# Optimization experiments

Measured on AMD Instinct MI355X. Metric: run time of the kernel, lower is better.

The kernel has to match this reference:

```python
import jax, jax.numpy as jnp
import numpy as np

HIDDEN = 1024
ATTN = 1024
B, L = 16, 1024


def setup_inputs() -> dict:
    key = jax.random.key(0)
    ks = jax.random.split(key, 9)
    s = 1.0 / np.sqrt(HIDDEN)
    return {
        "meme_features": jax.random.normal(ks[0], (B, L, HIDDEN), jnp.float32),
        "text_features": jax.random.normal(ks[1], (B, L, HIDDEN), jnp.float32),
        "emoji_features": jax.random.normal(ks[2], (B, L, HIDDEN), jnp.float32),
        # nn.Linear params: weight [out, in], bias [out]
        "Wq": jax.random.uniform(ks[3], (ATTN, HIDDEN), jnp.float32, -s, s),
        "bq": jax.random.uniform(ks[4], (ATTN,), jnp.float32, -s, s),
        "Wk": jax.random.uniform(ks[5], (ATTN, HIDDEN), jnp.float32, -s, s),
        "bk": jax.random.uniform(ks[6], (ATTN,), jnp.float32, -s, s),
        "Wv": jax.random.uniform(ks[7], (ATTN, HIDDEN), jnp.float32, -s, s),
        "bv": jax.random.uniform(ks[8], (ATTN,), jnp.float32, -s, s),
    }


def reference(meme_features, text_features, emoji_features, Wq, bq, Wk, bk, Wv, bv):
    # Linear projections (x @ W^T + b)
    q = jnp.einsum("blh,ah->bla", meme_features, Wq) + bq   # [B, Lq, A]
    k = jnp.einsum("blh,ah->bla", text_features, Wk) + bk   # [B, Lk, A]
    v = jnp.einsum("blh,ah->bla", emoji_features, Wv) + bv  # [B, Lk, A]
    # NOTE: original module has NO 1/sqrt(d) scaling and NO mask.
    scores = jnp.einsum("bqa,bka->bqk", q, k)               # [B, Lq, Lk]
    weights = jax.nn.softmax(scores, axis=-1)
    return jnp.einsum("bqk,bka->bqa", weights, v)           # [B, Lq, A]
```

## Files before the change

### kernel.cpp

```cpp
#include <hip/hip_runtime.h>

typedef _Float16 half8_t __attribute__((ext_vector_type(8)));
typedef _Float16 half4_t __attribute__((ext_vector_type(4)));
typedef float floatx4 __attribute__((ext_vector_type(4)));
typedef float f32x16 __attribute__((ext_vector_type(16)));

__device__ inline void gload16(const void* g, void* l) {
  __builtin_amdgcn_global_load_lds(
      (const __attribute__((address_space(1))) unsigned int*)g,
      (__attribute__((address_space(3))) unsigned int*)l, 16, 0, 0);
}

constexpr int NT = 16;

__device__ inline void lda_frags2(const char* sA, int rb, const int* xk,
                                  half8_t af[2][4]) {
#pragma unroll
  for (int mp = 0; mp < 2; ++mp)
#pragma unroll
    for (int ks = 0; ks < 4; ++ks)
      af[mp][ks] = *(const half8_t*)(
          sA + (size_t)((rb + mp * 32) * 128 + xk[ks] * 16));
}

__device__ inline void ldb_frags2(const char* sB, int cb, const int* xk,
                                  half8_t bf[4]) {
#pragma unroll
  for (int ks = 0; ks < 4; ++ks)
    bf[ks] = *(const half8_t*)(sB + (size_t)(cb * 128 + xk[ks] * 16));
}

template <int MQ, int NI>
__device__ inline void mfma_quad(const half8_t af[2][4], const half8_t bf[4],
                                 f32x16 acc[4][2]) {
  __builtin_amdgcn_s_setprio(1);
#pragma unroll
  for (int mp = 0; mp < 2; ++mp)
#pragma unroll
    for (int ks = 0; ks < 4; ++ks)
      acc[MQ + mp][NI] = __builtin_amdgcn_mfma_f32_32x32x16_f16(
          af[mp][ks], bf[ks], acc[MQ + mp][NI], 0, 0, 0);
  __builtin_amdgcn_s_setprio(0);
}

__device__ inline void stage_half(const _Float16* __restrict__ X, long laneoff,
                                  int ldx, int u, char* opbase, int h,
                                  int wid) {
#pragma unroll
  for (int i = 0; i < 2; ++i) {
    const int c0 = h * 1024 + wid * 128 + i * 64;
    gload16(X + (long)(c0 >> 3) * ldx + u * 64 + laneoff,
            opbase + (size_t)c0 * 16);
  }
}

template <typename OT, int BIAS, int GX, int GY>
__global__ __launch_bounds__(512, 2) void gemm256(
    const _Float16* __restrict__ A, long As, int lda,
    const _Float16* __restrict__ B, long Bs, int ldb,
    OT* __restrict__ C, long Cs, int ldc, const float* __restrict__ bias,
    int biasStride) {
  __shared__ char smem[131072];

  const int id = blockIdx.x;
  const int chunk = gridDim.x >> 3;
  const int nid = (id & 7) * chunk + (id >> 3);
  const int bx = nid % GX;
  const int by = (nid / GX) % GY;
  const int bz = nid / (GX * GY);

  const int tid = threadIdx.x;
  const int lane = tid & 63;
  const int wid = tid >> 6;
  const int wr = wid >> 2;
  const int wc = wid & 3;
  const int lo = lane & 31;
  const int hi = lane >> 5;
  const int l7 = lane & 7;
  const int l8 = lane >> 3;
  const long laneA = (long)l8 * lda + ((l7 ^ l8) << 3);
  const long laneB = (long)l8 * ldb + ((l7 ^ l8) << 3);
  int xk[4];
#pragma unroll
  for (int ks = 0; ks < 4; ++ks) xk[ks] = (ks * 2 + hi) ^ l7;

  const long m0 = (long)by * 256;
  const long n0 = (long)bx * 256;
  const _Float16* Ab = A + (long)bz * As + m0 * (long)lda;
  const _Float16* Bb = B + (long)bz * Bs + n0 * (long)ldb;
  C += (long)bz * Cs;

  f32x16 acc[4][2] = {};
  half8_t af[2][4], bf0[4], bf1[4];

  char* sA0 = smem;
  char* sA1 = smem + 32768;
  char* sB0 = smem + 65536;
  char* sB1 = smem + 65536 + 32768;

  stage_half(Ab, laneA, lda, 0, sA0, 0, wid);
  stage_half(Bb, laneB, ldb, 0, sB0, 1, wid);
  stage_half(Ab, laneA, lda, 0, sA0, 1, wid);
  stage_half(Bb, laneB, ldb, 0, sB0, 0, wid);
  stage_half(Ab, laneA, lda, 1, sA1, 0, wid);
  stage_half(Bb, laneB, ldb, 1, sB1, 1, wid);
  stage_half(Ab, laneA, lda, 1, sA1, 1, wid);
  asm volatile("s_waitcnt vmcnt(6)" ::: "memory");
  __builtin_amdgcn_s_barrier();

  for (int t = 0; t < NT; ++t) {
    const int p = t & 1, q = p ^ 1;
    char* sAc = smem + p * 32768;
    char* sBc = smem + 65536 + p * 32768;
    char* sBq = smem + 65536 + q * 32768;
    const int u1 = (t + 1 < NT) ? t + 1 : NT - 1;
    const int u2 = (t + 2 < NT) ? t + 2 : NT - 1;

    lda_frags2(sAc, wr * 64 + lo, xk, af);
    ldb_frags2(sBc, wc * 32 + lo, xk, bf0);
    stage_half(Bb, laneB, ldb, u1, sBq, 0, wid);
    __builtin_amdgcn_s_barrier();
    asm volatile("s_waitcnt lgkmcnt(0)" ::: "memory");
    mfma_quad<0, 0>(af, bf0, acc);
    __builtin_amdgcn_s_barrier();

    ldb_frags2(sBc, 128 + wc * 32 + lo, xk, bf1);
    stage_half(Ab, laneA, lda, u2, sAc, 0, wid);
    __builtin_amdgcn_s_barrier();
    asm volatile("s_waitcnt lgkmcnt(0)" ::: "memory");
    mfma_quad<0, 1>(af, bf1, acc);
    __builtin_amdgcn_s_barrier();

    lda_frags2(sAc, 128 + wr * 64 + lo, xk, af);
    stage_half(Bb, laneB, ldb, u2, sBc, 1, wid);
    __builtin_amdgcn_s_barrier();
    asm volatile("s_waitcnt lgkmcnt(0)" ::: "memory");
    mfma_quad<2, 1>(af, bf1, acc);
    __builtin_amdgcn_s_barrier();

    stage_half(Ab, laneA, lda, u2, sAc, 1, wid);
    asm volatile("s_waitcnt vmcnt(6)" ::: "memory");
    __builtin_amdgcn_s_barrier();
    asm volatile("s_waitcnt lgkmcnt(0)" ::: "memory");
    mfma_quad<2, 0>(af, bf0, acc);
    __builtin_amdgcn_s_barrier();
  }

  asm volatile("s_waitcnt vmcnt(0)" ::: "memory");

#pragma unroll
  for (int mi = 0; mi < 4; ++mi) {
    const int r0 = (mi >> 1) * 128 + wr * 64 + (mi & 1) * 32 + 4 * hi;
#pragma unroll
    for (int ni = 0; ni < 2; ++ni) {
      const int cc = (int)n0 + ni * 128 + wc * 32 + lo;
#pragma unroll
      for (int e = 0; e < 16; ++e) {
        const long row = m0 + r0 + (e & 3) + 8 * (e >> 2);
        float v = acc[mi][ni][e];
        if constexpr (BIAS == 1) v += bias[bz * biasStride + cc];
        if constexpr (BIAS == 2) v += bias[(int)row];
        C[row * (long)ldc + cc] = (OT)v;
      }
    }
  }
}


__global__ __launch_bounds__(256) void convert_x(const float* __restrict__ x0,
                                                 const float* __restrict__ x1,
                                                 const float* __restrict__ x2,
                                                 _Float16* __restrict__ out) {
  int i = blockIdx.x * 256 + threadIdx.x;
  int t = i >> 22;
  int j = i & 4194303;
  const float* src = (t == 0) ? x0 : (t == 1) ? x1 : x2;
  floatx4 v = ((const floatx4*)src)[j];
  half4_t h = {(_Float16)v[0], (_Float16)v[1], (_Float16)v[2], (_Float16)v[3]};
  ((half4_t*)out)[i] = h;
}

__global__ __launch_bounds__(256) void convert_w(const float* __restrict__ Wq,
                                                 const float* __restrict__ Wk,
                                                 const float* __restrict__ Wv,
                                                 _Float16* __restrict__ out) {
  int i = blockIdx.x * 256 + threadIdx.x;
  int t = i >> 18;
  int j = i & 262143;
  const float* src = (t == 0) ? Wq : (t == 1) ? Wk : Wv;
  floatx4 v = ((const floatx4*)src)[j];
  half4_t h = {(_Float16)v[0], (_Float16)v[1], (_Float16)v[2], (_Float16)v[3]};
  ((half4_t*)out)[i] = h;
}

__global__ __launch_bounds__(256) void pack_bias(const float* __restrict__ bq,
                                                 const float* __restrict__ bk,
                                                 const float* __restrict__ bv,
                                                 float* __restrict__ out) {
  int b = blockIdx.x;
  const float* src = (b == 0) ? bq : (b == 1) ? bk : bv;
  ((floatx4*)out)[b * 256 + threadIdx.x] =
      ((const floatx4*)src)[threadIdx.x];
}

__global__ __launch_bounds__(256) void softmax_rows_h(_Float16* __restrict__ S) {
  long row = blockIdx.x;
  _Float16* Sr = S + row * 1024;
  int tid = threadIdx.x, lane = tid & 63, wid = tid >> 6;
  half4_t x = ((const half4_t*)Sr)[tid];
  float x0 = x[0], x1 = x[1], x2 = x[2], x3 = x[3];
  float mx = fmaxf(fmaxf(x0, x1), fmaxf(x2, x3));
#pragma unroll
  for (int off = 32; off > 0; off >>= 1) mx = fmaxf(mx, __shfl_xor(mx, off));
  __shared__ float redm[4];
  if (lane == 0) redm[wid] = mx;
  __syncthreads();
  mx = fmaxf(fmaxf(redm[0], redm[1]), fmaxf(redm[2], redm[3]));
  float e0 = __expf(x0 - mx), e1 = __expf(x1 - mx);
  float e2 = __expf(x2 - mx), e3 = __expf(x3 - mx);
  float s = e0 + e1 + e2 + e3;
#pragma unroll
  for (int off = 32; off > 0; off >>= 1) s += __shfl_xor(s, off);
  __shared__ float reds[4];
  if (lane == 0) reds[wid] = s;
  __syncthreads();
  s = reds[0] + reds[1] + reds[2] + reds[3];
  float inv = 1.0f / s;
  half4_t h = {(_Float16)(e0 * inv), (_Float16)(e1 * inv),
               (_Float16)(e2 * inv), (_Float16)(e3 * inv)};
  ((half4_t*)Sr)[tid] = h;
}

extern "C" void kernel_launch(void* const* d_in, const int* in_sizes, int n_in,
                              void* d_out, int out_size, void* d_ws,
                              size_t ws_size, hipStream_t stream) {
  (void)in_sizes; (void)n_in; (void)out_size; (void)ws_size;
  const float* meme  = (const float*)d_in[0];
  const float* text  = (const float*)d_in[1];
  const float* emoji = (const float*)d_in[2];
  const float* Wq = (const float*)d_in[3];
  const float* bq = (const float*)d_in[4];
  const float* Wk = (const float*)d_in[5];
  const float* bk = (const float*)d_in[6];
  const float* Wv = (const float*)d_in[7];
  const float* bv = (const float*)d_in[8];

  const long MB = 1024 * 1024;
  char* ws = (char*)d_ws;
  _Float16* hWq = (_Float16*)ws;
  float* pbias  = (float*)(ws + 6 * MB);
  _Float16* mh  = (_Float16*)(ws + 7 * MB);
  _Float16* th  = (_Float16*)(ws + 39 * MB);
  _Float16* eh  = (_Float16*)(ws + 71 * MB);
  _Float16* Qh  = (_Float16*)(ws + 103 * MB);
  _Float16* Kh  = (_Float16*)(ws + 135 * MB);
  _Float16* S   = mh;
  _Float16* Vt  = th;
  _Float16* hWv = hWq + 2 * MB;

  dim3 blk(256), blk5(512);
  convert_w<<<3072, blk, 0, stream>>>(Wq, Wk, Wv, hWq);
  pack_bias<<<3, blk, 0, stream>>>(bq, bk, bv, pbias);
  convert_x<<<49152, blk, 0, stream>>>(meme, text, emoji, mh);

  gemm256<_Float16, 1, 4, 64><<<dim3(512), blk5, 0, stream>>>(
      mh, 16777216, 1024, hWq, 1048576, 1024, Qh, 16777216, 1024, pbias, 1024);
  gemm256<_Float16, 2, 64, 4><<<dim3(256), blk5, 0, stream>>>(
      hWv, 0, 1024, eh, 0, 1024, Vt, 0, 16384, pbias + 2048, 0);
  gemm256<_Float16, 0, 4, 4><<<dim3(256), blk5, 0, stream>>>(
      Qh, 1048576, 1024, Kh, 1048576, 1024, S, 1048576, 1024, nullptr, 0);
  softmax_rows_h<<<16384, blk, 0, stream>>>(S);
  gemm256<float, 0, 4, 4><<<dim3(256), blk5, 0, stream>>>(
      S, 1048576, 1024, Vt, 1024, 16384, (float*)d_out, 1048576, 1024,
      nullptr, 0);
}
```

Measured before the change: 444.9 us.

## Replace 256x256 eight-wave GEMM with simpler 128x128 four-wave double-buffered GEMM

```diff
diff --git a/kernel.cpp b/kernel.cpp
--- a/kernel.cpp
+++ b/kernel.cpp
@@ -13,8 +13,8 @@
 
 constexpr int NT = 16;
 
-__device__ inline void lda_frags2(const char* sA, int rb, const int* xk,
-                                  half8_t af[2][4]) {
+__device__ inline void lda_frags(const char* sA, int rb, const int* xk,
+                                 half8_t af[2][4]) {
 #pragma unroll
   for (int mp = 0; mp < 2; ++mp)
 #pragma unroll
@@ -23,44 +23,33 @@
           sA + (size_t)((rb + mp * 32) * 128 + xk[ks] * 16));
 }
 
-__device__ inline void ldb_frags2(const char* sB, int cb, const int* xk,
-                                  half8_t bf[4]) {
-#pragma unroll
-  for (int ks = 0; ks < 4; ++ks)
-    bf[ks] = *(const half8_t*)(sB + (size_t)(cb * 128 + xk[ks] * 16));
-}
-
-template <int MQ, int NI>
-__device__ inline void mfma_quad(const half8_t af[2][4], const half8_t bf[4],
-                                 f32x16 acc[4][2]) {
-  __builtin_amdgcn_s_setprio(1);
-#pragma unroll
-  for (int mp = 0; mp < 2; ++mp)
+__device__ inline void ldb_frags(const char* sB, int cb, const int* xk,
+                                 half8_t bf[2][4]) {
+#pragma unroll
+  for (int np = 0; np < 2; ++np)
 #pragma unroll
     for (int ks = 0; ks < 4; ++ks)
-      acc[MQ + mp][NI] = __builtin_amdgcn_mfma_f32_32x32x16_f16(
-          af[mp][ks], bf[ks], acc[MQ + mp][NI], 0, 0, 0);
-  __builtin_amdgcn_s_setprio(0);
-}
-
-__device__ inline void stage_half(const _Float16* __restrict__ X, long laneoff,
-                                  int ldx, int u, char* opbase, int h,
-                                  int wid) {
-#pragma unroll
-  for (int i = 0; i < 2; ++i) {
-    const int c0 = h * 1024 + wid * 128 + i * 64;
+      bf[np][ks] = *(const half8_t*)(
+          sB + (size_t)((cb + np * 32) * 128 + xk[ks] * 16));
+}
+
+__device__ inline void stage_op(const _Float16* __restrict__ X, long laneoff,
+                                int ldx, int u, char* opbase, int wid) {
+#pragma unroll
+  for (int j = 0; j < 4; ++j) {
+    const int c0 = (wid * 4 + j) * 64;
     gload16(X + (long)(c0 >> 3) * ldx + u * 64 + laneoff,
             opbase + (size_t)c0 * 16);
   }
 }
 
 template <typename OT, int BIAS, int GX, int GY>
-__global__ __launch_bounds__(512, 2) void gemm256(
+__global__ __launch_bounds__(256) void gemm128(
     const _Float16* __restrict__ A, long As, int lda,
     const _Float16* __restrict__ B, long Bs, int ldb,
     OT* __restrict__ C, long Cs, int ldc, const float* __restrict__ bias,
     int biasStride) {
-  __shared__ char smem[131072];
+  __shared__ char smem[65536];
 
   const int id = blockIdx.x;
   const int chunk = gridDim.x >> 3;
@@ -72,8 +61,8 @@
   const int tid = threadIdx.x;
   const int lane = tid & 63;
   const int wid = tid >> 6;
-  const int wr = wid >> 2;
-  const int wc = wid & 3;
+  const int wr = wid >> 1;
+  const int wc = wid & 1;
   const int lo = lane & 31;
   const int hi = lane >> 5;
   const int l7 = lane & 7;
@@ -84,80 +73,60 @@
 #pragma unroll
   for (int ks = 0; ks < 4; ++ks) xk[ks] = (ks * 2 + hi) ^ l7;
 
-  const long m0 = (long)by * 256;
-  const long n0 = (long)bx * 256;
+  const long m0 = (long)by * 128;
+  const long n0 = (long)bx * 128;
   const _Float16* Ab = A + (long)bz * As + m0 * (long)lda;
   const _Float16* Bb = B + (long)bz * Bs + n0 * (long)ldb;
   C += (long)bz * Cs;
 
-  f32x16 acc[4][2] = {};
-  half8_t af[2][4], bf0[4], bf1[4];
-
-  char* sA0 = smem;
-  char* sA1 = smem + 32768;
-  char* sB0 = smem + 65536;
-  char* sB1 = smem + 65536 + 32768;
-
-  stage_half(Ab, laneA, lda, 0, sA0, 0, wid);
-  stage_half(Bb, laneB, ldb, 0, sB0, 1, wid);
-  stage_half(Ab, laneA, lda, 0, sA0, 1, wid);
-  stage_half(Bb, laneB, ldb, 0, sB0, 0, wid);
-  stage_half(Ab, laneA, lda, 1, sA1, 0, wid);
-  stage_half(Bb, laneB, ldb, 1, sB1, 1, wid);
-  stage_half(Ab, laneA, lda, 1, sA1, 1, wid);
-  asm volatile("s_waitcnt vmcnt(6)" ::: "memory");
+  f32x16 acc[2][2] = {};
+  half8_t af[2][4], bf[2][4];
+
+  stage_op(Ab, laneA, lda, 0, smem, wid);
+  stage_op(Bb, laneB, ldb, 0, smem + 32768, wid);
+  asm volatile("s_waitcnt vmcnt(0)" ::: "memory");
   __builtin_amdgcn_s_barrier();
 
   for (int t = 0; t < NT; ++t) {
     const int p = t & 1, q = p ^ 1;
-    char* sAc = smem + p * 32768;
-    char* sBc = smem + 65536 + p * 32768;
-    char* sBq = smem + 65536 + q * 32768;
+    char* sAp = smem + p * 16384;
+    char* sBp = smem + 32768 + p * 16384;
+    char* sAq = smem + q * 16384;
+    char* sBq = smem + 32768 + q * 16384;
     const int u1 = (t + 1 < NT) ? t + 1 : NT - 1;
-    const int u2 = (t + 2 < NT) ? t + 2 : NT - 1;
-
-    lda_frags2(sAc, wr * 64 + lo, xk, af);
-    ldb_frags2(sBc, wc * 32 + lo, xk, bf0);
-    stage_half(Bb, laneB, ldb, u1, sBq, 0, wid);
-    __builtin_amdgcn_s_barrier();
+
+    stage_op(Ab, laneA, lda, u1, sAq, wid);
+    stage_op(Bb, laneB, ldb, u1, sBq, wid);
+
+    lda_frags(sAp, wr * 64 + lo, xk, af);
+    ldb_frags(sBp, wc * 64 + lo, xk, bf);
     asm volatile("s_waitcnt lgkmcnt(0)" ::: "memory");
-    mfma_quad<0, 0>(af, bf0, acc);
-    __builtin_amdgcn_s_barrier();
-
-    ldb_frags2(sBc, 128 + wc * 32 + lo, xk, bf1);
-    stage_half(Ab, laneA, lda, u2, sAc, 0, wid);
-    __builtin_amdgcn_s_barrier();
-    asm volatile("s_waitcnt lgkmcnt(0)" ::: "memory");
-    mfma_quad<0, 1>(af, bf1, acc);
-    __builtin_amdgcn_s_barrier();
-
-    lda_frags2(sAc, 128 + wr * 64 + lo, xk, af);
-    stage_half(Bb, laneB, ldb, u2, sBc, 1, wid);
-    __builtin_amdgcn_s_barrier();
-    asm volatile("s_waitcnt lgkmcnt(0)" ::: "memory");
-    mfma_quad<2, 1>(af, bf1, acc);
-    __builtin_amdgcn_s_barrier();
-
-    stage_half(Ab, laneA, lda, u2, sAc, 1, wid);
-    asm volatile("s_waitcnt vmcnt(6)" ::: "memory");
-    __builtin_amdgcn_s_barrier();
-    asm volatile("s_waitcnt lgkmcnt(0)" ::: "memory");
-    mfma_quad<2, 0>(af, bf0, acc);
+
+    __builtin_amdgcn_s_setprio(1);
+#pragma unroll
+    for (int mp = 0; mp < 2; ++mp)
+#pragma unroll
+      for (int np = 0; np < 2; ++np)
+#pragma unroll
+        for (int ks = 0; ks < 4; ++ks)
+          acc[mp][np] = __builtin_amdgcn_mfma_f32_32x32x16_f16(
+              af[mp][ks], bf[np][ks], acc[mp][np], 0, 0, 0);
+    __builtin_amdgcn_s_setprio(0);
+
+    asm volatile("s_waitcnt vmcnt(0)" ::: "memory");
     __builtin_amdgcn_s_barrier();
   }
 
-  asm volatile("s_waitcnt vmcnt(0)" ::: "memory");
-
-#pragma unroll
-  for (int mi = 0; mi < 4; ++mi) {
-    const int r0 = (mi >> 1) * 128 + wr * 64 + (mi & 1) * 32 + 4 * hi;
-#pragma unroll
-    for (int ni = 0; ni < 2; ++ni) {
-      const int cc = (int)n0 + ni * 128 + wc * 32 + lo;
+#pragma unroll
+  for (int mp = 0; mp < 2; ++mp) {
+    const int r0 = wr * 64 + mp * 32 + 4 * hi;
+#pragma unroll
+    for (int np = 0; np < 2; ++np) {
+      const int cc = (int)n0 + wc * 64 + np * 32 + lo;
 #pragma unroll
       for (int e = 0; e < 16; ++e) {
         const long row = m0 + r0 + (e & 3) + 8 * (e >> 2);
-        float v = acc[mi][ni][e];
+        float v = acc[mp][np][e];
         if constexpr (BIAS == 1) v += bias[bz * biasStride + cc];
         if constexpr (BIAS == 2) v += bias[(int)row];
         C[row * (long)ldc + cc] = (OT)v;
@@ -258,19 +227,19 @@
   _Float16* Vt  = th;
   _Float16* hWv = hWq + 2 * MB;
 
-  dim3 blk(256), blk5(512);
+  dim3 blk(256);
   convert_w<<<3072, blk, 0, stream>>>(Wq, Wk, Wv, hWq);
   pack_bias<<<3, blk, 0, stream>>>(bq, bk, bv, pbias);
   convert_x<<<49152, blk, 0, stream>>>(meme, text, emoji, mh);
 
-  gemm256<_Float16, 1, 4, 64><<<dim3(512), blk5, 0, stream>>>(
+  gemm128<_Float16, 1, 8, 128><<<dim3(2048), blk, 0, stream>>>(
       mh, 16777216, 1024, hWq, 1048576, 1024, Qh, 16777216, 1024, pbias, 1024);
-  gemm256<_Float16, 2, 64, 4><<<dim3(256), blk5, 0, stream>>>(
+  gemm128<_Float16, 2, 128, 8><<<dim3(1024), blk, 0, stream>>>(
       hWv, 0, 1024, eh, 0, 1024, Vt, 0, 16384, pbias + 2048, 0);
-  gemm256<_Float16, 0, 4, 4><<<dim3(256), blk5, 0, stream>>>(
+  gemm128<_Float16, 0, 8, 8><<<dim3(1024), blk, 0, stream>>>(
       Qh, 1048576, 1024, Kh, 1048576, 1024, S, 1048576, 1024, nullptr, 0);
   softmax_rows_h<<<16384, blk, 0, stream>>>(S);
-  gemm256<float, 0, 4, 4><<<dim3(256), blk5, 0, stream>>>(
+  gemm128<float, 0, 8, 8><<<dim3(1024), blk, 0, stream>>>(
       S, 1048576, 1024, Vt, 1024, 16384, (float*)d_out, 1048576, 1024,
       nullptr, 0);
 }
```

Measured after the change: 466.0 us. 4.8% more time.

## Load all LDS fragments up front and collapse the per-tile pipeline to two phases

Applied to the files above, without the earlier changes.

```diff
diff --git a/kernel.cpp b/kernel.cpp
--- a/kernel.cpp
+++ b/kernel.cpp
@@ -13,33 +13,38 @@
 
 constexpr int NT = 16;
 
-__device__ inline void lda_frags2(const char* sA, int rb, const int* xk,
-                                  half8_t af[2][4]) {
-#pragma unroll
-  for (int mp = 0; mp < 2; ++mp)
+__device__ inline void lda_all(const char* sA, int wr, int lo, const int* xk,
+                               half8_t af[4][4]) {
+#pragma unroll
+  for (int mi = 0; mi < 4; ++mi) {
+    const int row = (mi >> 1) * 128 + wr * 64 + (mi & 1) * 32 + lo;
 #pragma unroll
     for (int ks = 0; ks < 4; ++ks)
-      af[mp][ks] = *(const half8_t*)(
-          sA + (size_t)((rb + mp * 32) * 128 + xk[ks] * 16));
-}
-
-__device__ inline void ldb_frags2(const char* sB, int cb, const int* xk,
-                                  half8_t bf[4]) {
+      af[mi][ks] = *(const half8_t*)(sA + (size_t)(row * 128 + xk[ks] * 16));
+  }
+}
+
+__device__ inline void ldb_all(const char* sB, int wc, int lo, const int* xk,
+                               half8_t bf[2][4]) {
+#pragma unroll
+  for (int ni = 0; ni < 2; ++ni) {
+    const int row = ni * 128 + wc * 32 + lo;
+#pragma unroll
+    for (int ks = 0; ks < 4; ++ks)
+      bf[ni][ks] = *(const half8_t*)(sB + (size_t)(row * 128 + xk[ks] * 16));
+  }
+}
+
+template <int NI>
+__device__ inline void mfma_col(const half8_t af[4][4], const half8_t bf[2][4],
+                                f32x16 acc[4][2]) {
+  __builtin_amdgcn_s_setprio(1);
 #pragma unroll
   for (int ks = 0; ks < 4; ++ks)
-    bf[ks] = *(const half8_t*)(sB + (size_t)(cb * 128 + xk[ks] * 16));
-}
-
-template <int MQ, int NI>
-__device__ inline void mfma_quad(const half8_t af[2][4], const half8_t bf[4],
-                                 f32x16 acc[4][2]) {
-  __builtin_amdgcn_s_setprio(1);
-#pragma unroll
-  for (int mp = 0; mp < 2; ++mp)
-#pragma unroll
-    for (int ks = 0; ks < 4; ++ks)
-      acc[MQ + mp][NI] = __builtin_amdgcn_mfma_f32_32x32x16_f16(
-          af[mp][ks], bf[ks], acc[MQ + mp][NI], 0, 0, 0);
+#pragma unroll
+    for (int mi = 0; mi < 4; ++mi)
+      acc[mi][NI] = __builtin_amdgcn_mfma_f32_32x32x16_f16(
+          af[mi][ks], bf[NI][ks], acc[mi][NI], 0, 0, 0);
   __builtin_amdgcn_s_setprio(0);
 }
 
@@ -91,7 +96,7 @@
   C += (long)bz * Cs;
 
   f32x16 acc[4][2] = {};
-  half8_t af[2][4], bf0[4], bf1[4];
+  half8_t af[4][4], bf[2][4];
 
   char* sA0 = smem;
   char* sA1 = smem + 32768;
@@ -99,50 +104,36 @@
   char* sB1 = smem + 65536 + 32768;
 
   stage_half(Ab, laneA, lda, 0, sA0, 0, wid);
-  stage_half(Bb, laneB, ldb, 0, sB0, 1, wid);
   stage_half(Ab, laneA, lda, 0, sA0, 1, wid);
   stage_half(Bb, laneB, ldb, 0, sB0, 0, wid);
+  stage_half(Bb, laneB, ldb, 0, sB0, 1, wid);
   stage_half(Ab, laneA, lda, 1, sA1, 0, wid);
+  stage_half(Ab, laneA, lda, 1, sA1, 1, wid);
   stage_half(Bb, laneB, ldb, 1, sB1, 1, wid);
-  stage_half(Ab, laneA, lda, 1, sA1, 1, wid);
   asm volatile("s_waitcnt vmcnt(6)" ::: "memory");
   __builtin_amdgcn_s_barrier();
 
   for (int t = 0; t < NT; ++t) {
     const int p = t & 1, q = p ^ 1;
-    char* sAc = smem + p * 32768;
-    char* sBc = smem + 65536 + p * 32768;
+    char* sAp = smem + p * 32768;
+    char* sBp = smem + 65536 + p * 32768;
     char* sBq = smem + 65536 + q * 32768;
     const int u1 = (t + 1 < NT) ? t + 1 : NT - 1;
     const int u2 = (t + 2 < NT) ? t + 2 : NT - 1;
 
-    lda_frags2(sAc, wr * 64 + lo, xk, af);
-    ldb_frags2(sBc, wc * 32 + lo, xk, bf0);
+    lda_all(sAp, wr, lo, xk, af);
+    ldb_all(sBp, wc, lo, xk, bf);
     stage_half(Bb, laneB, ldb, u1, sBq, 0, wid);
     __builtin_amdgcn_s_barrier();
     asm volatile("s_waitcnt lgkmcnt(0)" ::: "memory");
-    mfma_quad<0, 0>(af, bf0, acc);
+    mfma_col<0>(af, bf, acc);
     __builtin_amdgcn_s_barrier();
 
-    ldb_frags2(sBc, 128 + wc * 32 + lo, xk, bf1);
-    stage_half(Ab, laneA, lda, u2, sAc, 0, wid);
-    __builtin_amdgcn_s_barrier();
-    asm volatile("s_waitcnt lgkmcnt(0)" ::: "memory");
-    mfma_quad<0, 1>(af, bf1, acc);
-    __builtin_amdgcn_s_barrier();
-
-    lda_frags2(sAc, 128 + wr * 64 + lo, xk, af);
-    stage_half(Bb, laneB, ldb, u2, sBc, 1, wid);
-    __builtin_amdgcn_s_barrier();
-    asm volatile("s_waitcnt lgkmcnt(0)" ::: "memory");
-    mfma_quad<2, 1>(af, bf1, acc);
-    __builtin_amdgcn_s_barrier();
-
-    stage_half(Ab, laneA, lda, u2, sAc, 1, wid);
+    stage_half(Ab, laneA, lda, u2, sAp, 0, wid);
+    stage_half(Ab, laneA, lda, u2, sAp, 1, wid);
+    stage_half(Bb, laneB, ldb, u2, sBp, 1, wid);
+    mfma_col<1>(af, bf, acc);
     asm volatile("s_waitcnt vmcnt(6)" ::: "memory");
-    __builtin_amdgcn_s_barrier();
-    asm volatile("s_waitcnt lgkmcnt(0)" ::: "memory");
-    mfma_quad<2, 0>(af, bf0, acc);
     __builtin_amdgcn_s_barrier();
   }
 
```

Result: slower. 472.3 us (+6.2%).

## Switch GEMM core to 16x16x32 MFMA with new LDS swizzle and staging order

Applied to the files above, without the earlier changes.

```diff
diff --git a/kernel.cpp b/kernel.cpp
--- a/kernel.cpp
+++ b/kernel.cpp
@@ -3,7 +3,6 @@
 typedef _Float16 half8_t __attribute__((ext_vector_type(8)));
 typedef _Float16 half4_t __attribute__((ext_vector_type(4)));
 typedef float floatx4 __attribute__((ext_vector_type(4)));
-typedef float f32x16 __attribute__((ext_vector_type(16)));
 
 __device__ inline void gload16(const void* g, void* l) {
   __builtin_amdgcn_global_load_lds(
@@ -13,45 +12,45 @@
 
 constexpr int NT = 16;
 
-__device__ inline void lda_frags2(const char* sA, int rb, const int* xk,
-                                  half8_t af[2][4]) {
-#pragma unroll
-  for (int mp = 0; mp < 2; ++mp)
-#pragma unroll
-    for (int ks = 0; ks < 4; ++ks)
-      af[mp][ks] = *(const half8_t*)(
-          sA + (size_t)((rb + mp * 32) * 128 + xk[ks] * 16));
-}
-
-__device__ inline void ldb_frags2(const char* sB, int cb, const int* xk,
-                                  half8_t bf[4]) {
-#pragma unroll
-  for (int ks = 0; ks < 4; ++ks)
-    bf[ks] = *(const half8_t*)(sB + (size_t)(cb * 128 + xk[ks] * 16));
-}
-
-template <int MQ, int NI>
-__device__ inline void mfma_quad(const half8_t af[2][4], const half8_t bf[4],
-                                 f32x16 acc[4][2]) {
+__device__ inline int swz(int row, int colbyte) {
+  return row * 128 + (colbyte ^ ((row & 6) << 3));
+}
+
+__device__ inline void lda8(const char* sAh, int kk, int l15, int l4,
+                            half8_t af[8]) {
+#pragma unroll
+  for (int mf = 0; mf < 8; ++mf)
+    af[mf] = *(const half8_t*)(sAh + swz(mf * 16 + l15, kk * 64 + l4 * 16));
+}
+
+__device__ inline void ldb2(const char* sBh, int rbase, int kk, int l15,
+                            int l4, half8_t bf[2]) {
+#pragma unroll
+  for (int nf = 0; nf < 2; ++nf)
+    bf[nf] = *(const half8_t*)(
+        sBh + swz(rbase + nf * 16 + l15, kk * 64 + l4 * 16));
+}
+
+template <int NP>
+__device__ inline void mfma16(const half8_t af[8], const half8_t bf[2],
+                              floatx4 acc[8][4]) {
   __builtin_amdgcn_s_setprio(1);
 #pragma unroll
-  for (int mp = 0; mp < 2; ++mp)
-#pragma unroll
-    for (int ks = 0; ks < 4; ++ks)
-      acc[MQ + mp][NI] = __builtin_amdgcn_mfma_f32_32x32x16_f16(
-          af[mp][ks], bf[ks], acc[MQ + mp][NI], 0, 0, 0);
+  for (int mf = 0; mf < 8; ++mf)
+#pragma unroll
+    for (int j = 0; j < 2; ++j)
+      acc[mf][NP * 2 + j] = __builtin_amdgcn_mfma_f32_16x16x32_f16(
+          af[mf], bf[j], acc[mf][NP * 2 + j], 0, 0, 0);
   __builtin_amdgcn_s_setprio(0);
 }
 
-__device__ inline void stage_half(const _Float16* __restrict__ X, long laneoff,
-                                  int ldx, int u, char* opbase, int h,
+__device__ inline void stage_half(const _Float16* __restrict__ Xh,
+                                  long laneoff, int ldx, int u, char* region,
                                   int wid) {
 #pragma unroll
-  for (int i = 0; i < 2; ++i) {
-    const int c0 = h * 1024 + wid * 128 + i * 64;
-    gload16(X + (long)(c0 >> 3) * ldx + u * 64 + laneoff,
-            opbase + (size_t)c0 * 16);
-  }
+  for (int i = 0; i < 2; ++i)
+    gload16(Xh + (long)(wid * 16 + i * 8) * ldx + u * 64 + laneoff,
+            region + (size_t)(wid * 2 + i) * 1024);
 }
 
 template <typename OT, int BIAS, int GX, int GY>
@@ -72,92 +71,95 @@
   const int tid = threadIdx.x;
   const int lane = tid & 63;
   const int wid = tid >> 6;
-  const int wr = wid >> 2;
-  const int wc = wid & 3;
-  const int lo = lane & 31;
-  const int hi = lane >> 5;
-  const int l7 = lane & 7;
-  const int l8 = lane >> 3;
-  const long laneA = (long)l8 * lda + ((l7 ^ l8) << 3);
-  const long laneB = (long)l8 * ldb + ((l7 ^ l8) << 3);
-  int xk[4];
-#pragma unroll
-  for (int ks = 0; ks < 4; ++ks) xk[ks] = (ks * 2 + hi) ^ l7;
+  const int wm = wid >> 2;
+  const int wn = wid & 3;
+  const int l15 = lane & 15;
+  const int l4 = lane >> 4;
+  const int brow = (wn & 1) * 64;
+  const int lperm = ((lane & 7) * 8) ^ (((lane >> 3) & 6) << 2);
+  const long laneA = (long)(lane >> 3) * lda + lperm;
+  const long laneB = (long)(lane >> 3) * ldb + lperm;
 
   const long m0 = (long)by * 256;
   const long n0 = (long)bx * 256;
   const _Float16* Ab = A + (long)bz * As + m0 * (long)lda;
   const _Float16* Bb = B + (long)bz * Bs + n0 * (long)ldb;
+  const _Float16* Ah0 = Ab;
+  const _Float16* Ah1 = Ab + 128 * (long)lda;
+  const _Float16* Bh0 = Bb;
+  const _Float16* Bh1 = Bb + 128 * (long)ldb;
   C += (long)bz * Cs;
 
-  f32x16 acc[4][2] = {};
-  half8_t af[2][4], bf0[4], bf1[4];
-
-  char* sA0 = smem;
-  char* sA1 = smem + 32768;
-  char* sB0 = smem + 65536;
-  char* sB1 = smem + 65536 + 32768;
-
-  stage_half(Ab, laneA, lda, 0, sA0, 0, wid);
-  stage_half(Bb, laneB, ldb, 0, sB0, 1, wid);
-  stage_half(Ab, laneA, lda, 0, sA0, 1, wid);
-  stage_half(Bb, laneB, ldb, 0, sB0, 0, wid);
-  stage_half(Ab, laneA, lda, 1, sA1, 0, wid);
-  stage_half(Bb, laneB, ldb, 1, sB1, 1, wid);
-  stage_half(Ab, laneA, lda, 1, sA1, 1, wid);
-  asm volatile("s_waitcnt vmcnt(6)" ::: "memory");
-  __builtin_amdgcn_s_barrier();
+  floatx4 acc[8][4] = {};
+  half8_t af[8], bf01[2], bf23[2];
+
+  {
+    char* p0 = smem;
+    char* p0b = smem + 65536;
+    stage_half(Ah0, laneA, lda, 0, p0, wid);
+    stage_half(Ah1, laneA, lda, 0, p0 + 16384, wid);
+    stage_half(Bh0, laneB, ldb, 0, p0b, wid);
+    stage_half(Bh1, laneB, ldb, 0, p0b + 16384, wid);
+    stage_half(Ah0, laneA, lda, 1, smem + 32768, wid);
+    asm volatile("s_waitcnt vmcnt(2)" ::: "memory");
+    __builtin_amdgcn_s_barrier();
+  }
 
   for (int t = 0; t < NT; ++t) {
     const int p = t & 1, q = p ^ 1;
-    char* sAc = smem + p * 32768;
-    char* sBc = smem + 65536 + p * 32768;
-    char* sBq = smem + 65536 + q * 32768;
+    char* pAbase = smem + p * 32768;
+    char* pBbase = smem + 65536 + p * 32768;
+    char* qAbase = smem + q * 32768;
+    char* qBbase = smem + 65536 + q * 32768;
+    const char* myA = pAbase + wm * 16384;
+    const char* myB = pBbase + (wn >> 1) * 16384;
     const int u1 = (t + 1 < NT) ? t + 1 : NT - 1;
     const int u2 = (t + 2 < NT) ? t + 2 : NT - 1;
 
-    lda_frags2(sAc, wr * 64 + lo, xk, af);
-    ldb_frags2(sBc, wc * 32 + lo, xk, bf0);
-    stage_half(Bb, laneB, ldb, u1, sBq, 0, wid);
-    __builtin_amdgcn_s_barrier();
-    asm volatile("s_waitcnt lgkmcnt(0)" ::: "memory");
-    mfma_quad<0, 0>(af, bf0, acc);
-    __builtin_amdgcn_s_barrier();
-
-    ldb_frags2(sBc, 128 + wc * 32 + lo, xk, bf1);
-    stage_half(Ab, laneA, lda, u2, sAc, 0, wid);
-    __builtin_amdgcn_s_barrier();
-    asm volatile("s_waitcnt lgkmcnt(0)" ::: "memory");
-    mfma_quad<0, 1>(af, bf1, acc);
-    __builtin_amdgcn_s_barrier();
-
-    lda_frags2(sAc, 128 + wr * 64 + lo, xk, af);
-    stage_half(Bb, laneB, ldb, u2, sBc, 1, wid);
-    __builtin_amdgcn_s_barrier();
-    asm volatile("s_waitcnt lgkmcnt(0)" ::: "memory");
-    mfma_quad<2, 1>(af, bf1, acc);
-    __builtin_amdgcn_s_barrier();
-
-    stage_half(Ab, laneA, lda, u2, sAc, 1, wid);
-    asm volatile("s_waitcnt vmcnt(6)" ::: "memory");
-    __builtin_amdgcn_s_barrier();
-    asm volatile("s_waitcnt lgkmcnt(0)" ::: "memory");
-    mfma_quad<2, 0>(af, bf0, acc);
+    lda8(myA, 0, l15, l4, af);
+    ldb2(myB, brow + 0, 0, l15, l4, bf01);
+    stage_half(Ah1, laneA, lda, u1, qAbase + 16384, wid);
+    __builtin_amdgcn_s_barrier();
+    asm volatile("s_waitcnt lgkmcnt(0)" ::: "memory");
+    mfma16<0>(af, bf01, acc);
+    __builtin_amdgcn_s_barrier();
+
+    ldb2(myB, brow + 32, 0, l15, l4, bf23);
+    stage_half(Bh0, laneB, ldb, u1, qBbase, wid);
+    __builtin_amdgcn_s_barrier();
+    asm volatile("s_waitcnt lgkmcnt(0)" ::: "memory");
+    mfma16<1>(af, bf23, acc);
+    __builtin_amdgcn_s_barrier();
+
+    lda8(myA, 1, l15, l4, af);
+    ldb2(myB, brow + 32, 1, l15, l4, bf23);
+    stage_half(Bh1, laneB, ldb, u1, qBbase + 16384, wid);
+    __builtin_amdgcn_s_barrier();
+    asm volatile("s_waitcnt lgkmcnt(0)" ::: "memory");
+    mfma16<1>(af, bf23, acc);
+    __builtin_amdgcn_s_barrier();
+
+    ldb2(myB, brow + 0, 1, l15, l4, bf01);
+    stage_half(Ah0, laneA, lda, u2, pAbase, wid);
+    asm volatile("s_waitcnt vmcnt(2)" ::: "memory");
+    __builtin_amdgcn_s_barrier();
+    asm volatile("s_waitcnt lgkmcnt(0)" ::: "memory");
+    mfma16<0>(af, bf01, acc);
     __builtin_amdgcn_s_barrier();
   }
 
   asm volatile("s_waitcnt vmcnt(0)" ::: "memory");
 
 #pragma unroll
-  for (int mi = 0; mi < 4; ++mi) {
-    const int r0 = (mi >> 1) * 128 + wr * 64 + (mi & 1) * 32 + 4 * hi;
-#pragma unroll
-    for (int ni = 0; ni < 2; ++ni) {
-      const int cc = (int)n0 + ni * 128 + wc * 32 + lo;
-#pragma unroll
-      for (int e = 0; e < 16; ++e) {
-        const long row = m0 + r0 + (e & 3) + 8 * (e >> 2);
-        float v = acc[mi][ni][e];
+  for (int mf = 0; mf < 8; ++mf) {
+    const int r0 = wm * 128 + mf * 16 + l4 * 4;
+#pragma unroll
+    for (int nf = 0; nf < 4; ++nf) {
+      const int cc = (int)n0 + wn * 64 + nf * 16 + l15;
+#pragma unroll
+      for (int r = 0; r < 4; ++r) {
+        const long row = m0 + r0 + r;
+        float v = acc[mf][nf][r];
         if constexpr (BIAS == 1) v += bias[bz * biasStride + cc];
         if constexpr (BIAS == 2) v += bias[(int)row];
         C[row * (long)ldc + cc] = (OT)v;
```

New measurement: 441.4 us. Within noise of the previous version (-0.8%).
